# Optimization experiments

Measured on AMD Instinct MI355X. Metric: run time of the kernel, lower is better.

Reference implementation:

```python
import jax, jax.numpy as jnp
import numpy as np

N = 50000        # num nodes
E = 600000       # num edges (before self-loops)
EPS = 1e-5       # BatchNorm eps


def _norm_coeffs(edge_index):
    # PyG GCNConv normalization: add self-loops, symmetric deg^-1/2 norm.
    loop = jnp.arange(N, dtype=edge_index.dtype)
    src = jnp.concatenate([edge_index[0], loop])
    dst = jnp.concatenate([edge_index[1], loop])
    deg = jax.ops.segment_sum(jnp.ones(src.shape[0], jnp.float32), dst, num_segments=N)
    dis = jax.lax.rsqrt(jnp.maximum(deg, 1.0))  # deg >= 1 due to self-loops
    norm = dis[src] * dis[dst]                  # [E+N]
    return src, dst, norm


def _gcn_layer(h, W, b, src, dst, norm):
    h = h @ W                                   # dense transform [N, out]
    msg = h[src] * norm[:, None]                # gather + scale  [E+N, out]
    agg = jax.ops.segment_sum(msg, dst, num_segments=N)  # scatter-add
    return agg + b


def _bn_relu(h, gamma, beta):
    mean = jnp.mean(h, axis=0)
    var = jnp.var(h, axis=0)
    h = (h - mean) * jax.lax.rsqrt(var + EPS) * gamma + beta
    return jax.nn.relu(h)


def setup_inputs() -> dict:
    key = jax.random.key(0)
    ks = jax.random.split(key, 5)
    x = jax.random.normal(ks[0], (N, 128), jnp.float32)
    edge_index = jax.random.randint(ks[1], (2, E), 0, N, jnp.int64)
    s = 0.05
    return {
        "x": x,
        "edge_index": edge_index,
        "W1": jax.random.normal(ks[2], (128, 128), jnp.float32) * s,
        "b1": jnp.zeros((128,), jnp.float32),
        "gamma1": jnp.ones((128,), jnp.float32),
        "beta1": jnp.zeros((128,), jnp.float32),
        "W2": jax.random.normal(ks[3], (128, 128), jnp.float32) * s,
        "b2": jnp.zeros((128,), jnp.float32),
        "gamma2": jnp.ones((128,), jnp.float32),
        "beta2": jnp.zeros((128,), jnp.float32),
        "W3": jax.random.normal(ks[4], (128, 64), jnp.float32) * s,
        "b3": jnp.zeros((64,), jnp.float32),
    }


def reference(x, edge_index, W1, b1, gamma1, beta1, W2, b2, gamma2, beta2, W3, b3):
    src, dst, norm = _norm_coeffs(edge_index)
    h = _gcn_layer(x, W1, b1, src, dst, norm)
    h = _bn_relu(h, gamma1, beta1)
    h = _gcn_layer(h, W2, b2, src, dst, norm)
    h = _bn_relu(h, gamma2, beta2)
    return _gcn_layer(h, W3, b3, src, dst, norm)
```

## Files before the change

### kernel.cpp

```cpp
#include <hip/hip_runtime.h>
#include <hip/hip_bf16.h>


#define NCHUNK 1024
#define NSLOT 64

typedef short bf16x8 __attribute__((ext_vector_type(8)));
typedef float f32x4 __attribute__((ext_vector_type(4)));

union FragU { uint4 u; bf16x8 f; };

static __device__ __forceinline__ float4 ld4(const float* p) {
    return *reinterpret_cast<const float4*>(p);
}

static __device__ __forceinline__ unsigned pk2(float lo, float hi) {
    __hip_bfloat162 h = __float22bfloat162_rn(make_float2(lo, hi));
    union { __hip_bfloat162 h2; unsigned u; } c;
    c.h2 = h;
    return c.u;
}
static __device__ __forceinline__ unsigned short bf1(float v) {
    return (unsigned short)(pk2(v, 0.f) & 0xffffu);
}
static __device__ __forceinline__ float bf_lo(unsigned u) { return __uint_as_float(u << 16); }
static __device__ __forceinline__ float bf_hi(unsigned u) { return __uint_as_float(u & 0xffff0000u); }

__global__ void k_init(int* __restrict__ cnt, float* __restrict__ stats, int n) {
    int i = blockIdx.x * 256 + threadIdx.x;
    if (i < n) cnt[i] = 0;
    if (i < 4 * NSLOT * 128) stats[i] = 0.f;
}

__global__ void k_count(const int* __restrict__ dst, int* __restrict__ cnt, int e) {
    int i = blockIdx.x * 256 + threadIdx.x;
    if (i < e) atomicAdd(&cnt[dst[i]], 1);
}

__global__ __launch_bounds__(256) void k_chunksum(const int* __restrict__ cnt,
                                                  int* __restrict__ chunkSum, int n) {
    int t = blockIdx.x * 256 + threadIdx.x;
    int per = (n + NCHUNK - 1) / NCHUNK;
    int lo = t * per; if (lo > n) lo = n;
    int hi = lo + per; if (hi > n) hi = n;
    int s = 0;
    for (int i = lo; i < hi; ++i) s += cnt[i];
    chunkSum[t] = s;
}

__global__ __launch_bounds__(256) void k_chunkwrite(const int* __restrict__ cnt,
                                                    const int* __restrict__ chunkSum,
                                                    int* __restrict__ offs,
                                                    int* __restrict__ cursor,
                                                    float* __restrict__ dis,
                                                    int n, int e) {
    __shared__ int lbase[NCHUNK];
    __shared__ int lth[256];
    int t = threadIdx.x;
    int a0 = chunkSum[t * 4 + 0], a1 = chunkSum[t * 4 + 1];
    int a2 = chunkSum[t * 4 + 2], a3 = chunkSum[t * 4 + 3];
    lth[t] = a0 + a1 + a2 + a3;
    __syncthreads();
    for (int off = 1; off < 256; off <<= 1) {
        int v = (t >= off) ? lth[t - off] : 0;
        __syncthreads();
        lth[t] += v;
        __syncthreads();
    }
    int base = (t == 0) ? 0 : lth[t - 1];
    lbase[t * 4 + 0] = base;
    lbase[t * 4 + 1] = base + a0;
    lbase[t * 4 + 2] = base + a0 + a1;
    lbase[t * 4 + 3] = base + a0 + a1 + a2;
    __syncthreads();
    int cid = blockIdx.x * 256 + t;
    int per = (n + NCHUNK - 1) / NCHUNK;
    int lo = cid * per; if (lo > n) lo = n;
    int hi = lo + per; if (hi > n) hi = n;
    int run = lbase[cid];
    for (int i = lo; i < hi; ++i) {
        offs[i] = run;
        cursor[i] = run;
        int c = cnt[i];
        dis[i] = rsqrtf((float)(c + 1));
        run += c;
    }
    if (cid == 0) offs[n] = e;
}

__global__ void k_scatter(const int* __restrict__ src, const int* __restrict__ dst,
                          int* __restrict__ cursor, int* __restrict__ csr, int e) {
    int i = blockIdx.x * 256 + threadIdx.x;
    if (i < e) {
        int p = atomicAdd(&cursor[dst[i]], 1);
        csr[p] = src[i];
    }
}

__global__ __launch_bounds__(64) void k_wprep3(const float* __restrict__ W1,
                                               const float* __restrict__ W2,
                                               const float* __restrict__ W3,
                                               unsigned short* __restrict__ wf1,
                                               unsigned short* __restrict__ wf2,
                                               unsigned short* __restrict__ wf3) {
    int b = blockIdx.x;
    const float* W; unsigned short* Wf; int NC; int blk;
    if (b < 32)      { W = W1; Wf = wf1; NC = 128; blk = b; }
    else if (b < 64) { W = W2; Wf = wf2; NC = 128; blk = b - 32; }
    else             { W = W3; Wf = wf3; NC = 64;  blk = b - 64; }
    int kk = blk & 3;
    int l = threadIdx.x;
    int col = (blk >> 2) * 16 + (l & 15);
    int k0 = kk * 32 + (l >> 4) * 8;
    unsigned short* dst = &Wf[((size_t)blk * 64 + l) * 8];
#pragma unroll
    for (int j = 0; j < 8; ++j)
        dst[j] = bf1(W[(size_t)(k0 + j) * NC + col]);
}

template <bool TRANS, int NC, bool INBF>
__global__ __launch_bounds__(256) void k_gemm(const void* __restrict__ inv,
                                              const uint4* __restrict__ Wf,
                                              const float* __restrict__ dis,
                                              const float* __restrict__ ta,
                                              const float* __restrict__ tc,
                                              unsigned short* __restrict__ out, int n) {
    constexpr int TPW = NC / 32;
    constexpr int PADC = NC + 8;
    constexpr int SHN = (32 * PADC > 32 * 128) ? 32 * PADC : 32 * 128;
    __shared__ unsigned short sh[SHN];
    const int tid = threadIdx.x;
    const int row0 = blockIdx.x * 32;

    if constexpr (INBF) {
        const unsigned short* in = (const unsigned short*)inv;
#pragma unroll
        for (int it = 0; it < 2; ++it) {
            int flat = it * 256 + tid;
            int r = flat >> 4, j = flat & 15;
            int grow = row0 + r;
            uint4 v = make_uint4(0, 0, 0, 0);
            if (grow < n) v = *reinterpret_cast<const uint4*>(&in[(size_t)grow * 128 + j * 8]);
            if (TRANS) {
                int f = j * 8;
                float4 A0 = ld4(&ta[f]), A1 = ld4(&ta[f + 4]);
                float4 C0 = ld4(&tc[f]), C1 = ld4(&tc[f + 4]);
                v.x = pk2(fmaxf(bf_lo(v.x) * A0.x + C0.x, 0.f),
                          fmaxf(bf_hi(v.x) * A0.y + C0.y, 0.f));
                v.y = pk2(fmaxf(bf_lo(v.y) * A0.z + C0.z, 0.f),
                          fmaxf(bf_hi(v.y) * A0.w + C0.w, 0.f));
                v.z = pk2(fmaxf(bf_lo(v.z) * A1.x + C1.x, 0.f),
                          fmaxf(bf_hi(v.z) * A1.y + C1.y, 0.f));
                v.w = pk2(fmaxf(bf_lo(v.w) * A1.z + C1.z, 0.f),
                          fmaxf(bf_hi(v.w) * A1.w + C1.w, 0.f));
            }
            int byte = r * 256 + ((j * 16) ^ ((r & 7) << 4));
            *reinterpret_cast<uint4*>(reinterpret_cast<char*>(sh) + byte) = v;
        }
    } else {
        const float* in = (const float*)inv;
#pragma unroll
        for (int it = 0; it < 4; ++it) {
            int flat = it * 256 + tid;
            int r = flat >> 5, j4 = flat & 31;
            int grow = row0 + r;
            float4 v = make_float4(0.f, 0.f, 0.f, 0.f);
            if (grow < n) v = ld4(&in[(size_t)grow * 128 + j4 * 4]);
            if (TRANS) {
                int f = j4 * 4;
                float4 A = ld4(&ta[f]);
                float4 C = ld4(&tc[f]);
                v.x = fmaxf(v.x * A.x + C.x, 0.f);
                v.y = fmaxf(v.y * A.y + C.y, 0.f);
                v.z = fmaxf(v.z * A.z + C.z, 0.f);
                v.w = fmaxf(v.w * A.w + C.w, 0.f);
            }
            int byte = r * 256 + ((j4 * 8) ^ ((r & 7) << 4));
            *reinterpret_cast<uint2*>(reinterpret_cast<char*>(sh) + byte) =
                make_uint2(pk2(v.x, v.y), pk2(v.z, v.w));
        }
    }
    __syncthreads();

    const int l = tid & 63, w = tid >> 6;
    const int l15 = l & 15, g = l >> 4;
    const int rhalf = (w >> 1) * 16;
    const int tbase = (w & 1) * TPW;

    f32x4 acc[TPW];
#pragma unroll
    for (int t = 0; t < TPW; ++t) acc[t] = (f32x4){0.f, 0.f, 0.f, 0.f};

    const int arow = rhalf + l15;
    const char* xb = reinterpret_cast<const char*>(sh) + arow * 256;
    const int aswz = (arow & 7) << 4;

#pragma unroll
    for (int kk = 0; kk < 4; ++kk) {
        FragU a;
        a.u = *reinterpret_cast<const uint4*>(xb + ((kk * 64 + g * 16) ^ aswz));
#pragma unroll
        for (int t = 0; t < TPW; ++t) {
            FragU b;
            b.u = Wf[(size_t)((tbase + t) * 4 + kk) * 64 + l];
            acc[t] = __builtin_amdgcn_mfma_f32_16x16x32_bf16(a.f, b.f, acc[t], 0, 0, 0);
        }
    }

    const int rbase = row0 + rhalf + g * 4;
    float dv[4];
#pragma unroll
    for (int r = 0; r < 4; ++r) {
        int rr = rbase + r;
        dv[r] = (rr < n) ? dis[rr] : 0.f;
    }
    __syncthreads();
#pragma unroll
    for (int t = 0; t < TPW; ++t) {
        int col = (tbase + t) * 16 + l15;
#pragma unroll
        for (int r = 0; r < 4; ++r) {
            int lrow = rhalf + g * 4 + r;
            sh[lrow * PADC + col] = bf1(acc[t][r] * dv[r]);
        }
    }
    __syncthreads();
    constexpr int U4R = NC / 8;
#pragma unroll
    for (int it = 0; it < (32 * U4R) / 256; ++it) {
        int flat = it * 256 + tid;
        int row = flat / U4R, j = flat % U4R;
        int grow = row0 + row;
        if (grow < n) {
            uint4 v = *reinterpret_cast<const uint4*>(&sh[row * PADC + j * 8]);
            *reinterpret_cast<uint4*>(&out[(size_t)grow * NC + j * 8]) = v;
        }
    }
}

template <int NC, bool STATS>
__global__ __launch_bounds__(256) void k_agg(const unsigned short* __restrict__ hs,
                                             const int* __restrict__ offs,
                                             const int* __restrict__ csr,
                                             const float* __restrict__ dis,
                                             const float* __restrict__ bias,
                                             void* __restrict__ outv,
                                             float* __restrict__ ssum,
                                             float* __restrict__ ssq, int n) {
    int wave = threadIdx.x >> 6, lane = threadIdx.x & 63;
    int node = blockIdx.x * 4 + wave;
    const int half = lane >> 5, l32 = lane & 31;

    if (NC == 128) {
        int e0 = 0, e1 = 0;
        if (node < n) { e0 = offs[node]; e1 = offs[node + 1]; }
        const uint2* hp = reinterpret_cast<const uint2*>(hs);
        float4 a0 = make_float4(0.f, 0.f, 0.f, 0.f);
        float4 a1 = a0, a2 = a0, a3 = a0;
        if (half == 0 && node < n) {
            uint2 w = hp[(size_t)node * 32 + l32];
            a0 = make_float4(bf_lo(w.x), bf_hi(w.x), bf_lo(w.y), bf_hi(w.y));
        }
        int e = e0;
        for (; e + 8 <= e1; e += 8) {
            int i0 = csr[e + 0 + half];
            int i1 = csr[e + 2 + half];
            int i2 = csr[e + 4 + half];
            int i3 = csr[e + 6 + half];
            uint2 w0 = hp[(size_t)i0 * 32 + l32];
            uint2 w1 = hp[(size_t)i1 * 32 + l32];
            uint2 w2 = hp[(size_t)i2 * 32 + l32];
            uint2 w3 = hp[(size_t)i3 * 32 + l32];
            a0.x += bf_lo(w0.x); a0.y += bf_hi(w0.x); a0.z += bf_lo(w0.y); a0.w += bf_hi(w0.y);
            a1.x += bf_lo(w1.x); a1.y += bf_hi(w1.x); a1.z += bf_lo(w1.y); a1.w += bf_hi(w1.y);
            a2.x += bf_lo(w2.x); a2.y += bf_hi(w2.x); a2.z += bf_lo(w2.y); a2.w += bf_hi(w2.y);
            a3.x += bf_lo(w3.x); a3.y += bf_hi(w3.x); a3.z += bf_lo(w3.y); a3.w += bf_hi(w3.y);
        }
        for (; e + 2 <= e1; e += 2) {
            int i0 = csr[e + half];
            uint2 w0 = hp[(size_t)i0 * 32 + l32];
            a0.x += bf_lo(w0.x); a0.y += bf_hi(w0.x); a0.z += bf_lo(w0.y); a0.w += bf_hi(w0.y);
        }
        if (e < e1 && half == 0) {
            int i0 = csr[e];
            uint2 w0 = hp[(size_t)i0 * 32 + l32];
            a0.x += bf_lo(w0.x); a0.y += bf_hi(w0.x); a0.z += bf_lo(w0.y); a0.w += bf_hi(w0.y);
        }
        a0.x += a1.x + a2.x + a3.x;
        a0.y += a1.y + a2.y + a3.y;
        a0.z += a1.z + a2.z + a3.z;
        a0.w += a1.w + a2.w + a3.w;
        a0.x += __shfl_down(a0.x, 32);
        a0.y += __shfl_down(a0.y, 32);
        a0.z += __shfl_down(a0.z, 32);
        a0.w += __shfl_down(a0.w, 32);
        float4 oV = make_float4(0.f, 0.f, 0.f, 0.f);
        if (half == 0 && node < n) {
            float d = dis[node];
            float4 b = ld4(&bias[l32 * 4]);
            oV = make_float4(d * a0.x + b.x, d * a0.y + b.y,
                             d * a0.z + b.z, d * a0.w + b.w);
            uint2 w = make_uint2(pk2(oV.x, oV.y), pk2(oV.z, oV.w));
            reinterpret_cast<uint2*>(outv)[(size_t)node * 32 + l32] = w;
        }
        if constexpr (STATS) {
            __shared__ float ls[4][128];
            __shared__ float ls2[4][128];
            if (half == 0) {
                int c = l32 * 4;
                ls[wave][c + 0] = oV.x; ls2[wave][c + 0] = oV.x * oV.x;
                ls[wave][c + 1] = oV.y; ls2[wave][c + 1] = oV.y * oV.y;
                ls[wave][c + 2] = oV.z; ls2[wave][c + 2] = oV.z * oV.z;
                ls[wave][c + 3] = oV.w; ls2[wave][c + 3] = oV.w * oV.w;
            }
            __syncthreads();
            int t = threadIdx.x;
            int slot = (blockIdx.x & (NSLOT - 1)) * 128;
            if (t < 128) {
                float s = ls[0][t] + ls[1][t] + ls[2][t] + ls[3][t];
                atomicAdd(&ssum[slot + t], s);
            } else {
                int c = t - 128;
                float s2 = ls2[0][c] + ls2[1][c] + ls2[2][c] + ls2[3][c];
                atomicAdd(&ssq[slot + c], s2);
            }
        }
    } else {
        if (node >= n) return;
        int e0 = offs[node], e1 = offs[node + 1];
        const unsigned* hp = reinterpret_cast<const unsigned*>(hs);
        float2 a0 = make_float2(0.f, 0.f);
        float2 a1 = a0, a2 = a0, a3 = a0;
        if (half == 0) {
            unsigned w = hp[(size_t)node * 32 + l32];
            a0 = make_float2(bf_lo(w), bf_hi(w));
        }
        int e = e0;
        for (; e + 8 <= e1; e += 8) {
            int i0 = csr[e + 0 + half];
            int i1 = csr[e + 2 + half];
            int i2 = csr[e + 4 + half];
            int i3 = csr[e + 6 + half];
            unsigned w0 = hp[(size_t)i0 * 32 + l32];
            unsigned w1 = hp[(size_t)i1 * 32 + l32];
            unsigned w2 = hp[(size_t)i2 * 32 + l32];
            unsigned w3 = hp[(size_t)i3 * 32 + l32];
            a0.x += bf_lo(w0); a0.y += bf_hi(w0);
            a1.x += bf_lo(w1); a1.y += bf_hi(w1);
            a2.x += bf_lo(w2); a2.y += bf_hi(w2);
            a3.x += bf_lo(w3); a3.y += bf_hi(w3);
        }
        for (; e + 2 <= e1; e += 2) {
            int i0 = csr[e + half];
            unsigned w0 = hp[(size_t)i0 * 32 + l32];
            a0.x += bf_lo(w0); a0.y += bf_hi(w0);
        }
        if (e < e1 && half == 0) {
            int i0 = csr[e];
            unsigned w0 = hp[(size_t)i0 * 32 + l32];
            a0.x += bf_lo(w0); a0.y += bf_hi(w0);
        }
        a0.x += a1.x + a2.x + a3.x;
        a0.y += a1.y + a2.y + a3.y;
        a0.x += __shfl_down(a0.x, 32);
        a0.y += __shfl_down(a0.y, 32);
        if (half == 0) {
            float d = dis[node];
            float2 o = make_float2(d * a0.x + bias[l32 * 2],
                                   d * a0.y + bias[l32 * 2 + 1]);
            reinterpret_cast<float2*>(outv)[(size_t)node * 32 + l32] = o;
        }
    }
}

__global__ void k_bnparams(const float* __restrict__ ssum, const float* __restrict__ ssq,
                           const float* __restrict__ gamma, const float* __restrict__ beta,
                           float* __restrict__ a, float* __restrict__ cc, int n) {
    int c = threadIdx.x;
    if (c < 128) {
        float s = 0.f, s2 = 0.f;
        for (int k = 0; k < NSLOT; ++k) {
            s += ssum[k * 128 + c];
            s2 += ssq[k * 128 + c];
        }
        float inv_n = 1.0f / (float)n;
        float mean = s * inv_n;
        float var = s2 * inv_n - mean * mean;
        float sc = gamma[c] * rsqrtf(var + 1e-5f);
        a[c] = sc;
        cc[c] = beta[c] - mean * sc;
    }
}

extern "C" void kernel_launch(void* const* d_in, const int* in_sizes, int n_in,
                              void* d_out, int out_size, void* d_ws, size_t ws_size,
                              hipStream_t stream) {
    const float* x      = (const float*)d_in[0];
    const int*   ei     = (const int*)d_in[1];
    const float* W1     = (const float*)d_in[2];
    const float* b1     = (const float*)d_in[3];
    const float* gamma1 = (const float*)d_in[4];
    const float* beta1  = (const float*)d_in[5];
    const float* W2     = (const float*)d_in[6];
    const float* b2     = (const float*)d_in[7];
    const float* gamma2 = (const float*)d_in[8];
    const float* beta2  = (const float*)d_in[9];
    const float* W3     = (const float*)d_in[10];
    const float* b3     = (const float*)d_in[11];
    float* out = (float*)d_out;

    const int n = in_sizes[0] / 128;
    const int e = in_sizes[1] / 2;
    const int* esrc = ei;
    const int* edst = ei + e;

    char* p = (char*)d_ws;
    auto alloc = [&](size_t bytes) {
        void* r = p;
        p += (bytes + 255) & ~size_t(255);
        return r;
    };
    unsigned short* hbf  = (unsigned short*)alloc(sizeof(unsigned short) * (size_t)n * 128);
    unsigned short* bufB = (unsigned short*)alloc(sizeof(unsigned short) * (size_t)n * 128);
    int*   cnt    = (int*)alloc(sizeof(int) * n);
    int*   offs   = (int*)alloc(sizeof(int) * (n + 1));
    int*   cursor = (int*)alloc(sizeof(int) * n);
    int*   csr    = (int*)alloc(sizeof(int) * e);
    float* dis    = (float*)alloc(sizeof(float) * n);
    float* stats  = (float*)alloc(sizeof(float) * 4 * NSLOT * 128);
    float* bn     = (float*)alloc(sizeof(float) * 512);
    int*   chunkSum  = (int*)alloc(sizeof(int) * NCHUNK);
    unsigned short* wf1 = (unsigned short*)alloc(sizeof(unsigned short) * 32 * 64 * 8);
    unsigned short* wf2 = (unsigned short*)alloc(sizeof(unsigned short) * 32 * 64 * 8);
    unsigned short* wf3 = (unsigned short*)alloc(sizeof(unsigned short) * 16 * 64 * 8);
    float* ssum1 = stats,                   *ssq1 = stats + NSLOT * 128;
    float* ssum2 = stats + 2 * NSLOT * 128, *ssq2 = stats + 3 * NSLOT * 128;
    float* a1 = bn, *cc1 = bn + 128, *a2 = bn + 256, *cc2 = bn + 384;

    int gb_n  = (n + 255) / 256;
    int gb_e  = (e + 255) / 256;
    int gb_gemm = (n + 31) / 32;
    int gb_agg = (n + 3) / 4;

    k_init<<<gb_n, 256, 0, stream>>>(cnt, stats, n);
    k_count<<<gb_e, 256, 0, stream>>>(edst, cnt, e);
    k_wprep3<<<80, 64, 0, stream>>>(W1, W2, W3, wf1, wf2, wf3);
    k_chunksum<<<NCHUNK / 256, 256, 0, stream>>>(cnt, chunkSum, n);
    k_chunkwrite<<<NCHUNK / 256, 256, 0, stream>>>(cnt, chunkSum, offs, cursor, dis, n, e);
    k_scatter<<<gb_e, 256, 0, stream>>>(esrc, edst, cursor, csr, e);

    k_gemm<false, 128, false><<<gb_gemm, 256, 0, stream>>>(x, (const uint4*)wf1, dis, nullptr, nullptr, hbf, n);
    k_agg<128, true><<<gb_agg, 256, 0, stream>>>(hbf, offs, csr, dis, b1, bufB, ssum1, ssq1, n);
    k_bnparams<<<1, 128, 0, stream>>>(ssum1, ssq1, gamma1, beta1, a1, cc1, n);

    k_gemm<true, 128, true><<<gb_gemm, 256, 0, stream>>>(bufB, (const uint4*)wf2, dis, a1, cc1, hbf, n);
    k_agg<128, true><<<gb_agg, 256, 0, stream>>>(hbf, offs, csr, dis, b2, bufB, ssum2, ssq2, n);
    k_bnparams<<<1, 128, 0, stream>>>(ssum2, ssq2, gamma2, beta2, a2, cc2, n);

    k_gemm<true, 64, true><<<gb_gemm, 256, 0, stream>>>(bufB, (const uint4*)wf3, dis, a2, cc2, hbf, n);
    k_agg<64, false><<<gb_agg, 256, 0, stream>>>(hbf, offs, csr, dis, b3, out, nullptr, nullptr, n);
}
```

Before: 243.6 us.

## Partition feature columns into 32-wide panels for cache-local gather aggregation

The GEMM epilogue now writes its bf16 output in a panel-major layout, with each 32-column slice stored contiguously across all nodes. The aggregation kernel gains a grid y-dimension over panels. Each wave gathers 64-byte rows from a single panel, so the working set per panel pass is smaller and more likely to stay in L2/MALL during random gathers. The trade-off is that csr and offs are re-read once per panel, and each wave now processes 8 edges per iteration with a shuffle reduction instead of unrolled accumulators.

```diff
diff --git a/kernel.cpp b/kernel.cpp
--- a/kernel.cpp
+++ b/kernel.cpp
@@ -233,12 +233,13 @@
         int grow = row0 + row;
         if (grow < n) {
             uint4 v = *reinterpret_cast<const uint4*>(&sh[row * PADC + j * 8]);
-            *reinterpret_cast<uint4*>(&out[(size_t)grow * NC + j * 8]) = v;
-        }
-    }
-}
-
-template <int NC, bool STATS>
+            int pp = j >> 2, pj = j & 3;
+            *reinterpret_cast<uint4*>(&out[((size_t)pp * n + grow) * 32 + pj * 8]) = v;
+        }
+    }
+}
+
+template <int OC, bool STATS, bool OUTF32>
 __global__ __launch_bounds__(256) void k_agg(const unsigned short* __restrict__ hs,
                                              const int* __restrict__ offs,
                                              const int* __restrict__ csr,
@@ -247,128 +248,64 @@
                                              void* __restrict__ outv,
                                              float* __restrict__ ssum,
                                              float* __restrict__ ssq, int n) {
-    int wave = threadIdx.x >> 6, lane = threadIdx.x & 63;
-    int node = blockIdx.x * 4 + wave;
-    const int half = lane >> 5, l32 = lane & 31;
-
-    if (NC == 128) {
-        int e0 = 0, e1 = 0;
-        if (node < n) { e0 = offs[node]; e1 = offs[node + 1]; }
-        const uint2* hp = reinterpret_cast<const uint2*>(hs);
-        float4 a0 = make_float4(0.f, 0.f, 0.f, 0.f);
-        float4 a1 = a0, a2 = a0, a3 = a0;
-        if (half == 0 && node < n) {
-            uint2 w = hp[(size_t)node * 32 + l32];
-            a0 = make_float4(bf_lo(w.x), bf_hi(w.x), bf_lo(w.y), bf_hi(w.y));
-        }
-        int e = e0;
-        for (; e + 8 <= e1; e += 8) {
-            int i0 = csr[e + 0 + half];
-            int i1 = csr[e + 2 + half];
-            int i2 = csr[e + 4 + half];
-            int i3 = csr[e + 6 + half];
-            uint2 w0 = hp[(size_t)i0 * 32 + l32];
-            uint2 w1 = hp[(size_t)i1 * 32 + l32];
-            uint2 w2 = hp[(size_t)i2 * 32 + l32];
-            uint2 w3 = hp[(size_t)i3 * 32 + l32];
-            a0.x += bf_lo(w0.x); a0.y += bf_hi(w0.x); a0.z += bf_lo(w0.y); a0.w += bf_hi(w0.y);
-            a1.x += bf_lo(w1.x); a1.y += bf_hi(w1.x); a1.z += bf_lo(w1.y); a1.w += bf_hi(w1.y);
-            a2.x += bf_lo(w2.x); a2.y += bf_hi(w2.x); a2.z += bf_lo(w2.y); a2.w += bf_hi(w2.y);
-            a3.x += bf_lo(w3.x); a3.y += bf_hi(w3.x); a3.z += bf_lo(w3.y); a3.w += bf_hi(w3.y);
-        }
-        for (; e + 2 <= e1; e += 2) {
-            int i0 = csr[e + half];
-            uint2 w0 = hp[(size_t)i0 * 32 + l32];
-            a0.x += bf_lo(w0.x); a0.y += bf_hi(w0.x); a0.z += bf_lo(w0.y); a0.w += bf_hi(w0.y);
-        }
-        if (e < e1 && half == 0) {
-            int i0 = csr[e];
-            uint2 w0 = hp[(size_t)i0 * 32 + l32];
-            a0.x += bf_lo(w0.x); a0.y += bf_hi(w0.x); a0.z += bf_lo(w0.y); a0.w += bf_hi(w0.y);
-        }
-        a0.x += a1.x + a2.x + a3.x;
-        a0.y += a1.y + a2.y + a3.y;
-        a0.z += a1.z + a2.z + a3.z;
-        a0.w += a1.w + a2.w + a3.w;
-        a0.x += __shfl_down(a0.x, 32);
-        a0.y += __shfl_down(a0.y, 32);
-        a0.z += __shfl_down(a0.z, 32);
-        a0.w += __shfl_down(a0.w, 32);
-        float4 oV = make_float4(0.f, 0.f, 0.f, 0.f);
-        if (half == 0 && node < n) {
-            float d = dis[node];
-            float4 b = ld4(&bias[l32 * 4]);
-            oV = make_float4(d * a0.x + b.x, d * a0.y + b.y,
-                             d * a0.z + b.z, d * a0.w + b.w);
+    const int wave = threadIdx.x >> 6, lane = threadIdx.x & 63;
+    const int node = blockIdx.x * 4 + wave;
+    const int p = blockIdx.y;
+    const int g = lane >> 3, li = lane & 7;
+    const uint2* hp = reinterpret_cast<const uint2*>(hs) + (size_t)p * n * 8;
+
+    int e0 = 0, e1 = 0;
+    if (node < n) { e0 = offs[node]; e1 = offs[node + 1]; }
+
+    float4 acc = make_float4(0.f, 0.f, 0.f, 0.f);
+    if (node < n && g == 0) {
+        uint2 w = hp[(size_t)node * 8 + li];
+        acc = make_float4(bf_lo(w.x), bf_hi(w.x), bf_lo(w.y), bf_hi(w.y));
+    }
+    for (int e = e0; e + g < e1; e += 8) {
+        int idx = csr[e + g];
+        uint2 w = hp[(size_t)idx * 8 + li];
+        acc.x += bf_lo(w.x); acc.y += bf_hi(w.x);
+        acc.z += bf_lo(w.y); acc.w += bf_hi(w.y);
+    }
+#pragma unroll
+    for (int off = 8; off < 64; off <<= 1) {
+        acc.x += __shfl_down(acc.x, off);
+        acc.y += __shfl_down(acc.y, off);
+        acc.z += __shfl_down(acc.z, off);
+        acc.w += __shfl_down(acc.w, off);
+    }
+    float4 oV = make_float4(0.f, 0.f, 0.f, 0.f);
+    if (node < n && g == 0) {
+        float d = dis[node];
+        float4 b = ld4(&bias[p * 32 + li * 4]);
+        oV = make_float4(d * acc.x + b.x, d * acc.y + b.y,
+                         d * acc.z + b.z, d * acc.w + b.w);
+        if constexpr (OUTF32) {
+            reinterpret_cast<float4*>(outv)[(size_t)node * (OC / 4) + p * 8 + li] = oV;
+        } else {
             uint2 w = make_uint2(pk2(oV.x, oV.y), pk2(oV.z, oV.w));
-            reinterpret_cast<uint2*>(outv)[(size_t)node * 32 + l32] = w;
-        }
-        if constexpr (STATS) {
-            __shared__ float ls[4][128];
-            __shared__ float ls2[4][128];
-            if (half == 0) {
-                int c = l32 * 4;
-                ls[wave][c + 0] = oV.x; ls2[wave][c + 0] = oV.x * oV.x;
-                ls[wave][c + 1] = oV.y; ls2[wave][c + 1] = oV.y * oV.y;
-                ls[wave][c + 2] = oV.z; ls2[wave][c + 2] = oV.z * oV.z;
-                ls[wave][c + 3] = oV.w; ls2[wave][c + 3] = oV.w * oV.w;
-            }
-            __syncthreads();
-            int t = threadIdx.x;
-            int slot = (blockIdx.x & (NSLOT - 1)) * 128;
-            if (t < 128) {
-                float s = ls[0][t] + ls[1][t] + ls[2][t] + ls[3][t];
-                atomicAdd(&ssum[slot + t], s);
-            } else {
-                int c = t - 128;
-                float s2 = ls2[0][c] + ls2[1][c] + ls2[2][c] + ls2[3][c];
-                atomicAdd(&ssq[slot + c], s2);
-            }
-        }
-    } else {
-        if (node >= n) return;
-        int e0 = offs[node], e1 = offs[node + 1];
-        const unsigned* hp = reinterpret_cast<const unsigned*>(hs);
-        float2 a0 = make_float2(0.f, 0.f);
-        float2 a1 = a0, a2 = a0, a3 = a0;
-        if (half == 0) {
-            unsigned w = hp[(size_t)node * 32 + l32];
-            a0 = make_float2(bf_lo(w), bf_hi(w));
-        }
-        int e = e0;
-        for (; e + 8 <= e1; e += 8) {
-            int i0 = csr[e + 0 + half];
-            int i1 = csr[e + 2 + half];
-            int i2 = csr[e + 4 + half];
-            int i3 = csr[e + 6 + half];
-            unsigned w0 = hp[(size_t)i0 * 32 + l32];
-            unsigned w1 = hp[(size_t)i1 * 32 + l32];
-            unsigned w2 = hp[(size_t)i2 * 32 + l32];
-            unsigned w3 = hp[(size_t)i3 * 32 + l32];
-            a0.x += bf_lo(w0); a0.y += bf_hi(w0);
-            a1.x += bf_lo(w1); a1.y += bf_hi(w1);
-            a2.x += bf_lo(w2); a2.y += bf_hi(w2);
-            a3.x += bf_lo(w3); a3.y += bf_hi(w3);
-        }
-        for (; e + 2 <= e1; e += 2) {
-            int i0 = csr[e + half];
-            unsigned w0 = hp[(size_t)i0 * 32 + l32];
-            a0.x += bf_lo(w0); a0.y += bf_hi(w0);
-        }
-        if (e < e1 && half == 0) {
-            int i0 = csr[e];
-            unsigned w0 = hp[(size_t)i0 * 32 + l32];
-            a0.x += bf_lo(w0); a0.y += bf_hi(w0);
-        }
-        a0.x += a1.x + a2.x + a3.x;
-        a0.y += a1.y + a2.y + a3.y;
-        a0.x += __shfl_down(a0.x, 32);
-        a0.y += __shfl_down(a0.y, 32);
-        if (half == 0) {
-            float d = dis[node];
-            float2 o = make_float2(d * a0.x + bias[l32 * 2],
-                                   d * a0.y + bias[l32 * 2 + 1]);
-            reinterpret_cast<float2*>(outv)[(size_t)node * 32 + l32] = o;
+            reinterpret_cast<uint2*>(outv)[(size_t)node * (OC / 4) + p * 8 + li] = w;
+        }
+    }
+    if constexpr (STATS) {
+        __shared__ float ls[4][32];
+        __shared__ float ls2[4][32];
+        if (g == 0) {
+            int c = li * 4;
+            ls[wave][c + 0] = oV.x; ls2[wave][c + 0] = oV.x * oV.x;
+            ls[wave][c + 1] = oV.y; ls2[wave][c + 1] = oV.y * oV.y;
+            ls[wave][c + 2] = oV.z; ls2[wave][c + 2] = oV.z * oV.z;
+            ls[wave][c + 3] = oV.w; ls2[wave][c + 3] = oV.w * oV.w;
+        }
+        __syncthreads();
+        int t = threadIdx.x;
+        int slot = (blockIdx.x & (NSLOT - 1)) * 128 + p * 32;
+        if (t < 32) {
+            atomicAdd(&ssum[slot + t], ls[0][t] + ls[1][t] + ls[2][t] + ls[3][t]);
+        } else if (t < 64) {
+            int c = t - 32;
+            atomicAdd(&ssq[slot + c], ls2[0][c] + ls2[1][c] + ls2[2][c] + ls2[3][c]);
         }
     }
 }
@@ -440,7 +377,8 @@
     int gb_n  = (n + 255) / 256;
     int gb_e  = (e + 255) / 256;
     int gb_gemm = (n + 31) / 32;
-    int gb_agg = (n + 3) / 4;
+    dim3 gb_agg4((n + 3) / 4, 4);
+    dim3 gb_agg2((n + 3) / 4, 2);
 
     k_init<<<gb_n, 256, 0, stream>>>(cnt, stats, n);
     k_count<<<gb_e, 256, 0, stream>>>(edst, cnt, e);
@@ -450,13 +388,13 @@
     k_scatter<<<gb_e, 256, 0, stream>>>(esrc, edst, cursor, csr, e);
 
     k_gemm<false, 128, false><<<gb_gemm, 256, 0, stream>>>(x, (const uint4*)wf1, dis, nullptr, nullptr, hbf, n);
-    k_agg<128, true><<<gb_agg, 256, 0, stream>>>(hbf, offs, csr, dis, b1, bufB, ssum1, ssq1, n);
+    k_agg<128, true, false><<<gb_agg4, 256, 0, stream>>>(hbf, offs, csr, dis, b1, bufB, ssum1, ssq1, n);
     k_bnparams<<<1, 128, 0, stream>>>(ssum1, ssq1, gamma1, beta1, a1, cc1, n);
 
     k_gemm<true, 128, true><<<gb_gemm, 256, 0, stream>>>(bufB, (const uint4*)wf2, dis, a1, cc1, hbf, n);
-    k_agg<128, true><<<gb_agg, 256, 0, stream>>>(hbf, offs, csr, dis, b2, bufB, ssum2, ssq2, n);
+    k_agg<128, true, false><<<gb_agg4, 256, 0, stream>>>(hbf, offs, csr, dis, b2, bufB, ssum2, ssq2, n);
     k_bnparams<<<1, 128, 0, stream>>>(ssum2, ssq2, gamma2, beta2, a2, cc2, n);
 
     k_gemm<true, 64, true><<<gb_gemm, 256, 0, stream>>>(bufB, (const uint4*)wf3, dis, a2, cc2, hbf, n);
-    k_agg<64, false><<<gb_agg, 256, 0, stream>>>(hbf, offs, csr, dis, b3, out, nullptr, nullptr, n);
-}
+    k_agg<64, false, true><<<gb_agg2, 256, 0, stream>>>(hbf, offs, csr, dis, b3, out, nullptr, nullptr, n);
+}
```

After: 336.4 us. +38.1%, slower.

## Merge setup kernels and process several nodes per wave in aggregation

Applied to the files above, without the earlier changes.

Folds the init and weight-prep kernels into one launch, and merges the chunk-sum pass into the chunk-write kernel so each block recomputes chunk sums redundantly. This removes two kernel launches. The aggregation kernel now handles four nodes per wave and accumulates BN statistics in registers, cutting the per-block shared-memory reduction and atomic traffic by four. The cost is fewer blocks in aggregation, which may reduce latency hiding, and redundant cnt reads in each chunk-write block.

```diff
diff --git a/kernel.cpp b/kernel.cpp
--- a/kernel.cpp
+++ b/kernel.cpp
@@ -4,6 +4,7 @@
 
 #define NCHUNK 1024
 #define NSLOT 64
+#define NPW 4
 
 typedef short bf16x8 __attribute__((ext_vector_type(8)));
 typedef float f32x4 __attribute__((ext_vector_type(4)));
@@ -26,10 +27,36 @@
 static __device__ __forceinline__ float bf_lo(unsigned u) { return __uint_as_float(u << 16); }
 static __device__ __forceinline__ float bf_hi(unsigned u) { return __uint_as_float(u & 0xffff0000u); }
 
-__global__ void k_init(int* __restrict__ cnt, float* __restrict__ stats, int n) {
-    int i = blockIdx.x * 256 + threadIdx.x;
-    if (i < n) cnt[i] = 0;
-    if (i < 4 * NSLOT * 128) stats[i] = 0.f;
+__global__ __launch_bounds__(256) void k_setup(int* __restrict__ cnt,
+                                               float* __restrict__ stats, int n,
+                                               int gbInit,
+                                               const float* __restrict__ W1,
+                                               const float* __restrict__ W2,
+                                               const float* __restrict__ W3,
+                                               unsigned short* __restrict__ wf1,
+                                               unsigned short* __restrict__ wf2,
+                                               unsigned short* __restrict__ wf3) {
+    int b = blockIdx.x;
+    if (b < gbInit) {
+        int i = b * 256 + threadIdx.x;
+        if (i < n) cnt[i] = 0;
+        if (i < 4 * NSLOT * 128) stats[i] = 0.f;
+        return;
+    }
+    int unit = (b - gbInit) * 4 + (threadIdx.x >> 6);
+    if (unit >= 80) return;
+    int l = threadIdx.x & 63;
+    const float* W; unsigned short* Wf; int NC; int blk;
+    if (unit < 32)      { W = W1; Wf = wf1; NC = 128; blk = unit; }
+    else if (unit < 64) { W = W2; Wf = wf2; NC = 128; blk = unit - 32; }
+    else                { W = W3; Wf = wf3; NC = 64;  blk = unit - 64; }
+    int kk = blk & 3;
+    int col = (blk >> 2) * 16 + (l & 15);
+    int k0 = kk * 32 + (l >> 4) * 8;
+    unsigned short* dst = &Wf[((size_t)blk * 64 + l) * 8];
+#pragma unroll
+    for (int j = 0; j < 8; ++j)
+        dst[j] = bf1(W[(size_t)(k0 + j) * NC + col]);
 }
 
 __global__ void k_count(const int* __restrict__ dst, int* __restrict__ cnt, int e) {
@@ -37,19 +64,7 @@
     if (i < e) atomicAdd(&cnt[dst[i]], 1);
 }
 
-__global__ __launch_bounds__(256) void k_chunksum(const int* __restrict__ cnt,
-                                                  int* __restrict__ chunkSum, int n) {
-    int t = blockIdx.x * 256 + threadIdx.x;
-    int per = (n + NCHUNK - 1) / NCHUNK;
-    int lo = t * per; if (lo > n) lo = n;
-    int hi = lo + per; if (hi > n) hi = n;
-    int s = 0;
-    for (int i = lo; i < hi; ++i) s += cnt[i];
-    chunkSum[t] = s;
-}
-
 __global__ __launch_bounds__(256) void k_chunkwrite(const int* __restrict__ cnt,
-                                                    const int* __restrict__ chunkSum,
                                                     int* __restrict__ offs,
                                                     int* __restrict__ cursor,
                                                     float* __restrict__ dis,
@@ -57,9 +72,20 @@
     __shared__ int lbase[NCHUNK];
     __shared__ int lth[256];
     int t = threadIdx.x;
-    int a0 = chunkSum[t * 4 + 0], a1 = chunkSum[t * 4 + 1];
-    int a2 = chunkSum[t * 4 + 2], a3 = chunkSum[t * 4 + 3];
-    lth[t] = a0 + a1 + a2 + a3;
+    int per = (n + NCHUNK - 1) / NCHUNK;
+    int cs[4];
+    int th = 0;
+#pragma unroll
+    for (int q = 0; q < 4; ++q) {
+        int cid = t * 4 + q;
+        int lo = cid * per; if (lo > n) lo = n;
+        int hi = lo + per; if (hi > n) hi = n;
+        int s = 0;
+        for (int i = lo; i < hi; ++i) s += cnt[i];
+        cs[q] = s;
+        th += s;
+    }
+    lth[t] = th;
     __syncthreads();
     for (int off = 1; off < 256; off <<= 1) {
         int v = (t >= off) ? lth[t - off] : 0;
@@ -69,12 +95,11 @@
     }
     int base = (t == 0) ? 0 : lth[t - 1];
     lbase[t * 4 + 0] = base;
-    lbase[t * 4 + 1] = base + a0;
-    lbase[t * 4 + 2] = base + a0 + a1;
-    lbase[t * 4 + 3] = base + a0 + a1 + a2;
+    lbase[t * 4 + 1] = base + cs[0];
+    lbase[t * 4 + 2] = base + cs[0] + cs[1];
+    lbase[t * 4 + 3] = base + cs[0] + cs[1] + cs[2];
     __syncthreads();
     int cid = blockIdx.x * 256 + t;
-    int per = (n + NCHUNK - 1) / NCHUNK;
     int lo = cid * per; if (lo > n) lo = n;
     int hi = lo + per; if (hi > n) hi = n;
     int run = lbase[cid];
@@ -95,27 +120,6 @@
         int p = atomicAdd(&cursor[dst[i]], 1);
         csr[p] = src[i];
     }
-}
-
-__global__ __launch_bounds__(64) void k_wprep3(const float* __restrict__ W1,
-                                               const float* __restrict__ W2,
-                                               const float* __restrict__ W3,
-                                               unsigned short* __restrict__ wf1,
-                                               unsigned short* __restrict__ wf2,
-                                               unsigned short* __restrict__ wf3) {
-    int b = blockIdx.x;
-    const float* W; unsigned short* Wf; int NC; int blk;
-    if (b < 32)      { W = W1; Wf = wf1; NC = 128; blk = b; }
-    else if (b < 64) { W = W2; Wf = wf2; NC = 128; blk = b - 32; }
-    else             { W = W3; Wf = wf3; NC = 64;  blk = b - 64; }
-    int kk = blk & 3;
-    int l = threadIdx.x;
-    int col = (blk >> 2) * 16 + (l & 15);
-    int k0 = kk * 32 + (l >> 4) * 8;
-    unsigned short* dst = &Wf[((size_t)blk * 64 + l) * 8];
-#pragma unroll
-    for (int j = 0; j < 8; ++j)
-        dst[j] = bf1(W[(size_t)(k0 + j) * NC + col]);
 }
 
 template <bool TRANS, int NC, bool INBF>
@@ -247,128 +251,137 @@
                                              void* __restrict__ outv,
                                              float* __restrict__ ssum,
                                              float* __restrict__ ssq, int n) {
-    int wave = threadIdx.x >> 6, lane = threadIdx.x & 63;
-    int node = blockIdx.x * 4 + wave;
+    const int wave = threadIdx.x >> 6, lane = threadIdx.x & 63;
     const int half = lane >> 5, l32 = lane & 31;
-
-    if (NC == 128) {
+    const int nodeBase = blockIdx.x * (4 * NPW) + wave * NPW;
+
+    float4 st = make_float4(0.f, 0.f, 0.f, 0.f);
+    float4 sq = make_float4(0.f, 0.f, 0.f, 0.f);
+
+    for (int j = 0; j < NPW; ++j) {
+        const int node = nodeBase + j;
         int e0 = 0, e1 = 0;
         if (node < n) { e0 = offs[node]; e1 = offs[node + 1]; }
-        const uint2* hp = reinterpret_cast<const uint2*>(hs);
-        float4 a0 = make_float4(0.f, 0.f, 0.f, 0.f);
-        float4 a1 = a0, a2 = a0, a3 = a0;
-        if (half == 0 && node < n) {
-            uint2 w = hp[(size_t)node * 32 + l32];
-            a0 = make_float4(bf_lo(w.x), bf_hi(w.x), bf_lo(w.y), bf_hi(w.y));
-        }
-        int e = e0;
-        for (; e + 8 <= e1; e += 8) {
-            int i0 = csr[e + 0 + half];
-            int i1 = csr[e + 2 + half];
-            int i2 = csr[e + 4 + half];
-            int i3 = csr[e + 6 + half];
-            uint2 w0 = hp[(size_t)i0 * 32 + l32];
-            uint2 w1 = hp[(size_t)i1 * 32 + l32];
-            uint2 w2 = hp[(size_t)i2 * 32 + l32];
-            uint2 w3 = hp[(size_t)i3 * 32 + l32];
-            a0.x += bf_lo(w0.x); a0.y += bf_hi(w0.x); a0.z += bf_lo(w0.y); a0.w += bf_hi(w0.y);
-            a1.x += bf_lo(w1.x); a1.y += bf_hi(w1.x); a1.z += bf_lo(w1.y); a1.w += bf_hi(w1.y);
-            a2.x += bf_lo(w2.x); a2.y += bf_hi(w2.x); a2.z += bf_lo(w2.y); a2.w += bf_hi(w2.y);
-            a3.x += bf_lo(w3.x); a3.y += bf_hi(w3.x); a3.z += bf_lo(w3.y); a3.w += bf_hi(w3.y);
-        }
-        for (; e + 2 <= e1; e += 2) {
-            int i0 = csr[e + half];
-            uint2 w0 = hp[(size_t)i0 * 32 + l32];
-            a0.x += bf_lo(w0.x); a0.y += bf_hi(w0.x); a0.z += bf_lo(w0.y); a0.w += bf_hi(w0.y);
-        }
-        if (e < e1 && half == 0) {
-            int i0 = csr[e];
-            uint2 w0 = hp[(size_t)i0 * 32 + l32];
-            a0.x += bf_lo(w0.x); a0.y += bf_hi(w0.x); a0.z += bf_lo(w0.y); a0.w += bf_hi(w0.y);
-        }
-        a0.x += a1.x + a2.x + a3.x;
-        a0.y += a1.y + a2.y + a3.y;
-        a0.z += a1.z + a2.z + a3.z;
-        a0.w += a1.w + a2.w + a3.w;
-        a0.x += __shfl_down(a0.x, 32);
-        a0.y += __shfl_down(a0.y, 32);
-        a0.z += __shfl_down(a0.z, 32);
-        a0.w += __shfl_down(a0.w, 32);
-        float4 oV = make_float4(0.f, 0.f, 0.f, 0.f);
-        if (half == 0 && node < n) {
-            float d = dis[node];
-            float4 b = ld4(&bias[l32 * 4]);
-            oV = make_float4(d * a0.x + b.x, d * a0.y + b.y,
-                             d * a0.z + b.z, d * a0.w + b.w);
-            uint2 w = make_uint2(pk2(oV.x, oV.y), pk2(oV.z, oV.w));
-            reinterpret_cast<uint2*>(outv)[(size_t)node * 32 + l32] = w;
-        }
-        if constexpr (STATS) {
-            __shared__ float ls[4][128];
-            __shared__ float ls2[4][128];
-            if (half == 0) {
-                int c = l32 * 4;
-                ls[wave][c + 0] = oV.x; ls2[wave][c + 0] = oV.x * oV.x;
-                ls[wave][c + 1] = oV.y; ls2[wave][c + 1] = oV.y * oV.y;
-                ls[wave][c + 2] = oV.z; ls2[wave][c + 2] = oV.z * oV.z;
-                ls[wave][c + 3] = oV.w; ls2[wave][c + 3] = oV.w * oV.w;
-            }
-            __syncthreads();
-            int t = threadIdx.x;
-            int slot = (blockIdx.x & (NSLOT - 1)) * 128;
-            if (t < 128) {
-                float s = ls[0][t] + ls[1][t] + ls[2][t] + ls[3][t];
-                atomicAdd(&ssum[slot + t], s);
-            } else {
-                int c = t - 128;
-                float s2 = ls2[0][c] + ls2[1][c] + ls2[2][c] + ls2[3][c];
-                atomicAdd(&ssq[slot + c], s2);
-            }
-        }
-    } else {
-        if (node >= n) return;
-        int e0 = offs[node], e1 = offs[node + 1];
-        const unsigned* hp = reinterpret_cast<const unsigned*>(hs);
-        float2 a0 = make_float2(0.f, 0.f);
-        float2 a1 = a0, a2 = a0, a3 = a0;
+
+        if (NC == 128) {
+            const uint2* hp = reinterpret_cast<const uint2*>(hs);
+            float4 a0 = make_float4(0.f, 0.f, 0.f, 0.f);
+            float4 a1 = a0, a2 = a0, a3 = a0;
+            if (half == 0 && node < n) {
+                uint2 w = hp[(size_t)node * 32 + l32];
+                a0 = make_float4(bf_lo(w.x), bf_hi(w.x), bf_lo(w.y), bf_hi(w.y));
+            }
+            int e = e0;
+            for (; e + 8 <= e1; e += 8) {
+                int i0 = csr[e + 0 + half];
+                int i1 = csr[e + 2 + half];
+                int i2 = csr[e + 4 + half];
+                int i3 = csr[e + 6 + half];
+                uint2 w0 = hp[(size_t)i0 * 32 + l32];
+                uint2 w1 = hp[(size_t)i1 * 32 + l32];
+                uint2 w2 = hp[(size_t)i2 * 32 + l32];
+                uint2 w3 = hp[(size_t)i3 * 32 + l32];
+                a0.x += bf_lo(w0.x); a0.y += bf_hi(w0.x); a0.z += bf_lo(w0.y); a0.w += bf_hi(w0.y);
+                a1.x += bf_lo(w1.x); a1.y += bf_hi(w1.x); a1.z += bf_lo(w1.y); a1.w += bf_hi(w1.y);
+                a2.x += bf_lo(w2.x); a2.y += bf_hi(w2.x); a2.z += bf_lo(w2.y); a2.w += bf_hi(w2.y);
+                a3.x += bf_lo(w3.x); a3.y += bf_hi(w3.x); a3.z += bf_lo(w3.y); a3.w += bf_hi(w3.y);
+            }
+            for (; e + 2 <= e1; e += 2) {
+                int i0 = csr[e + half];
+                uint2 w0 = hp[(size_t)i0 * 32 + l32];
+                a0.x += bf_lo(w0.x); a0.y += bf_hi(w0.x); a0.z += bf_lo(w0.y); a0.w += bf_hi(w0.y);
+            }
+            if (e < e1 && half == 0) {
+                int i0 = csr[e];
+                uint2 w0 = hp[(size_t)i0 * 32 + l32];
+                a0.x += bf_lo(w0.x); a0.y += bf_hi(w0.x); a0.z += bf_lo(w0.y); a0.w += bf_hi(w0.y);
+            }
+            a0.x += a1.x + a2.x + a3.x;
+            a0.y += a1.y + a2.y + a3.y;
+            a0.z += a1.z + a2.z + a3.z;
+            a0.w += a1.w + a2.w + a3.w;
+            a0.x += __shfl_down(a0.x, 32);
+            a0.y += __shfl_down(a0.y, 32);
+            a0.z += __shfl_down(a0.z, 32);
+            a0.w += __shfl_down(a0.w, 32);
+            if (half == 0 && node < n) {
+                float d = dis[node];
+                float4 b = ld4(&bias[l32 * 4]);
+                float4 oV = make_float4(d * a0.x + b.x, d * a0.y + b.y,
+                                        d * a0.z + b.z, d * a0.w + b.w);
+                uint2 w = make_uint2(pk2(oV.x, oV.y), pk2(oV.z, oV.w));
+                reinterpret_cast<uint2*>(outv)[(size_t)node * 32 + l32] = w;
+                if (STATS) {
+                    st.x += oV.x; sq.x += oV.x * oV.x;
+                    st.y += oV.y; sq.y += oV.y * oV.y;
+                    st.z += oV.z; sq.z += oV.z * oV.z;
+                    st.w += oV.w; sq.w += oV.w * oV.w;
+                }
+            }
+        } else {
+            const unsigned* hp = reinterpret_cast<const unsigned*>(hs);
+            float2 a0 = make_float2(0.f, 0.f);
+            float2 a1 = a0, a2 = a0, a3 = a0;
+            if (half == 0 && node < n) {
+                unsigned w = hp[(size_t)node * 32 + l32];
+                a0 = make_float2(bf_lo(w), bf_hi(w));
+            }
+            int e = e0;
+            for (; e + 8 <= e1; e += 8) {
+                int i0 = csr[e + 0 + half];
+                int i1 = csr[e + 2 + half];
+                int i2 = csr[e + 4 + half];
+                int i3 = csr[e + 6 + half];
+                unsigned w0 = hp[(size_t)i0 * 32 + l32];
+                unsigned w1 = hp[(size_t)i1 * 32 + l32];
+                unsigned w2 = hp[(size_t)i2 * 32 + l32];
+                unsigned w3 = hp[(size_t)i3 * 32 + l32];
+                a0.x += bf_lo(w0); a0.y += bf_hi(w0);
+                a1.x += bf_lo(w1); a1.y += bf_hi(w1);
+                a2.x += bf_lo(w2); a2.y += bf_hi(w2);
+                a3.x += bf_lo(w3); a3.y += bf_hi(w3);
+            }
+            for (; e + 2 <= e1; e += 2) {
+                int i0 = csr[e + half];
+                unsigned w0 = hp[(size_t)i0 * 32 + l32];
+                a0.x += bf_lo(w0); a0.y += bf_hi(w0);
+            }
+            if (e < e1 && half == 0) {
+                int i0 = csr[e];
+                unsigned w0 = hp[(size_t)i0 * 32 + l32];
+                a0.x += bf_lo(w0); a0.y += bf_hi(w0);
+            }
+            a0.x += a1.x + a2.x + a3.x;
+            a0.y += a1.y + a2.y + a3.y;
+            a0.x += __shfl_down(a0.x, 32);
+            a0.y += __shfl_down(a0.y, 32);
+            if (half == 0 && node < n) {
+                float d = dis[node];
+                float2 o = make_float2(d * a0.x + bias[l32 * 2],
+                                       d * a0.y + bias[l32 * 2 + 1]);
+                reinterpret_cast<float2*>(outv)[(size_t)node * 32 + l32] = o;
+            }
+        }
+    }
+
+    if constexpr (STATS) {
+        __shared__ float ls[4][128];
+        __shared__ float ls2[4][128];
         if (half == 0) {
-            unsigned w = hp[(size_t)node * 32 + l32];
-            a0 = make_float2(bf_lo(w), bf_hi(w));
-        }
-        int e = e0;
-        for (; e + 8 <= e1; e += 8) {
-            int i0 = csr[e + 0 + half];
-            int i1 = csr[e + 2 + half];
-            int i2 = csr[e + 4 + half];
-            int i3 = csr[e + 6 + half];
-            unsigned w0 = hp[(size_t)i0 * 32 + l32];
-            unsigned w1 = hp[(size_t)i1 * 32 + l32];
-            unsigned w2 = hp[(size_t)i2 * 32 + l32];
-            unsigned w3 = hp[(size_t)i3 * 32 + l32];
-            a0.x += bf_lo(w0); a0.y += bf_hi(w0);
-            a1.x += bf_lo(w1); a1.y += bf_hi(w1);
-            a2.x += bf_lo(w2); a2.y += bf_hi(w2);
-            a3.x += bf_lo(w3); a3.y += bf_hi(w3);
-        }
-        for (; e + 2 <= e1; e += 2) {
-            int i0 = csr[e + half];
-            unsigned w0 = hp[(size_t)i0 * 32 + l32];
-            a0.x += bf_lo(w0); a0.y += bf_hi(w0);
-        }
-        if (e < e1 && half == 0) {
-            int i0 = csr[e];
-            unsigned w0 = hp[(size_t)i0 * 32 + l32];
-            a0.x += bf_lo(w0); a0.y += bf_hi(w0);
-        }
-        a0.x += a1.x + a2.x + a3.x;
-        a0.y += a1.y + a2.y + a3.y;
-        a0.x += __shfl_down(a0.x, 32);
-        a0.y += __shfl_down(a0.y, 32);
-        if (half == 0) {
-            float d = dis[node];
-            float2 o = make_float2(d * a0.x + bias[l32 * 2],
-                                   d * a0.y + bias[l32 * 2 + 1]);
-            reinterpret_cast<float2*>(outv)[(size_t)node * 32 + l32] = o;
+            int c = l32 * 4;
+            ls[wave][c + 0] = st.x; ls2[wave][c + 0] = sq.x;
+            ls[wave][c + 1] = st.y; ls2[wave][c + 1] = sq.y;
+            ls[wave][c + 2] = st.z; ls2[wave][c + 2] = sq.z;
+            ls[wave][c + 3] = st.w; ls2[wave][c + 3] = sq.w;
+        }
+        __syncthreads();
+        int t = threadIdx.x;
+        int slot = (blockIdx.x & (NSLOT - 1)) * 128;
+        if (t < 128) {
+            atomicAdd(&ssum[slot + t], ls[0][t] + ls[1][t] + ls[2][t] + ls[3][t]);
+        } else {
+            int c = t - 128;
+            atomicAdd(&ssq[slot + c], ls2[0][c] + ls2[1][c] + ls2[2][c] + ls2[3][c]);
         }
     }
 }
@@ -429,7 +442,6 @@
     float* dis    = (float*)alloc(sizeof(float) * n);
     float* stats  = (float*)alloc(sizeof(float) * 4 * NSLOT * 128);
     float* bn     = (float*)alloc(sizeof(float) * 512);
-    int*   chunkSum  = (int*)alloc(sizeof(int) * NCHUNK);
     unsigned short* wf1 = (unsigned short*)alloc(sizeof(unsigned short) * 32 * 64 * 8);
     unsigned short* wf2 = (unsigned short*)alloc(sizeof(unsigned short) * 32 * 64 * 8);
     unsigned short* wf3 = (unsigned short*)alloc(sizeof(unsigned short) * 16 * 64 * 8);
@@ -440,13 +452,11 @@
     int gb_n  = (n + 255) / 256;
     int gb_e  = (e + 255) / 256;
     int gb_gemm = (n + 31) / 32;
-    int gb_agg = (n + 3) / 4;
-
-    k_init<<<gb_n, 256, 0, stream>>>(cnt, stats, n);
+    int gb_agg = (n + 4 * NPW - 1) / (4 * NPW);
+
+    k_setup<<<gb_n + 20, 256, 0, stream>>>(cnt, stats, n, gb_n, W1, W2, W3, wf1, wf2, wf3);
     k_count<<<gb_e, 256, 0, stream>>>(edst, cnt, e);
-    k_wprep3<<<80, 64, 0, stream>>>(W1, W2, W3, wf1, wf2, wf3);
-    k_chunksum<<<NCHUNK / 256, 256, 0, stream>>>(cnt, chunkSum, n);
-    k_chunkwrite<<<NCHUNK / 256, 256, 0, stream>>>(cnt, chunkSum, offs, cursor, dis, n, e);
+    k_chunkwrite<<<NCHUNK / 256, 256, 0, stream>>>(cnt, offs, cursor, dis, n, e);
     k_scatter<<<gb_e, 256, 0, stream>>>(esrc, edst, cursor, csr, e);
 
     k_gemm<false, 128, false><<<gb_gemm, 256, 0, stream>>>(x, (const uint4*)wf1, dis, nullptr, nullptr, hbf, n);
```

Result: slower. 265.2 us (+8.8%).
